# Performance work log

Measured on AMD Instinct MI355X. Metric: run time of the kernel, lower is better.

The kernel has to match this reference:

```python
import jax, jax.numpy as jnp
import numpy as np

OUT_FEATURES = 4096
IN_FEATURES = 4096
NUMEL = OUT_FEATURES * IN_FEATURES          # 16777216
NUM_SUPER = NUMEL // 256                    # 65536 superblocks of 256 weights


def setup_inputs() -> dict:
    key = jax.random.key(0)
    k_x, k_p, k_d, k_dm, k_s, k_m = jax.random.split(key, 6)
    x = jax.random.normal(k_x, (2, 2048, IN_FEATURES), dtype=jnp.float32)
    # packed bytes: two 4-bit quants per byte
    packed = jax.random.randint(k_p, (NUMEL // 2,), 0, 256, dtype=jnp.int32)
    # per-superblock fp scale/min (small positive values like real Q4_K 'd'/'dmin')
    d = jax.random.uniform(k_d, (NUM_SUPER,), dtype=jnp.float32) * 0.02
    dmin = jax.random.uniform(k_dm, (NUM_SUPER,), dtype=jnp.float32) * 0.02
    # per-subblock 6-bit scale/min quants (8 subblocks per superblock)
    scales = jax.random.randint(k_s, (NUM_SUPER * 8,), 0, 64, dtype=jnp.int32)
    mins = jax.random.randint(k_m, (NUM_SUPER * 8,), 0, 64, dtype=jnp.int32)
    return {"x": x, "packed": packed, "d": d, "dmin": dmin,
            "scales": scales, "mins": mins}


def _q4_k_dequantize(packed, d, dmin, scales, mins):
    # nibble split: low then high, interleaved per byte (stack dim=1 + flatten)
    low = packed & 15
    high = (packed >> 4) & 15
    q = jnp.stack([low, high], axis=1).reshape(-1).astype(jnp.float32)  # [NUMEL]
    blocks = q.reshape(NUM_SUPER, 8, 32)
    blk_scale = (scales.astype(jnp.float32) / 63.0).reshape(NUM_SUPER, 8, 1)
    blk_min = (mins.astype(jnp.float32) / 63.0).reshape(NUM_SUPER, 8, 1)
    normalized = blocks / 15.0 * blk_scale + blk_min
    w = normalized * d.reshape(NUM_SUPER, 1, 1) + dmin.reshape(NUM_SUPER, 1, 1)
    return w.reshape(OUT_FEATURES, IN_FEATURES)


def reference(x, packed, d, dmin, scales, mins):
    w = _q4_k_dequantize(packed, d, dmin, scales, mins).astype(x.dtype)
    # F.linear(x, w) = x @ w.T ; bias is None
    return jnp.einsum('bsk,nk->bsn', x, w)
```

## Files before the change

### kernel.cpp

```cpp
#include <hip/hip_runtime.h>
#include <stdint.h>

#define M_DIM 4096
#define K_DIM 4096
#define N_DIM 4096

typedef float f32x4 __attribute__((ext_vector_type(4)));
typedef int   i32x4 __attribute__((ext_vector_type(4)));

__global__ __launch_bounds__(256) void quant_x(const float* __restrict__ x,
                                               int8_t* __restrict__ xq,
                                               float* __restrict__ sx) {
    __shared__ float red[4];
    const int row  = blockIdx.x;
    const int base = threadIdx.x * 16;
    const float* xr = x + (size_t)row * K_DIM + base;
    float4 v[4];
#pragma unroll
    for (int c = 0; c < 4; ++c) v[c] = ((const float4*)xr)[c];
    float am = 0.f;
#pragma unroll
    for (int c = 0; c < 4; ++c) {
        am = fmaxf(am, fabsf(v[c].x)); am = fmaxf(am, fabsf(v[c].y));
        am = fmaxf(am, fabsf(v[c].z)); am = fmaxf(am, fabsf(v[c].w));
    }
#pragma unroll
    for (int off = 32; off; off >>= 1) am = fmaxf(am, __shfl_xor(am, off, 64));
    if ((threadIdx.x & 63) == 0) red[threadIdx.x >> 6] = am;
    __syncthreads();
    float amax = fmaxf(fmaxf(red[0], red[1]), fmaxf(red[2], red[3]));
    amax = fmaxf(amax, 1e-20f);
    const float inv = 127.0f / amax;
    int ow[4];
#pragma unroll
    for (int c = 0; c < 4; ++c) {
        int q0 = __float2int_rn(v[c].x * inv);
        int q1 = __float2int_rn(v[c].y * inv);
        int q2 = __float2int_rn(v[c].z * inv);
        int q3 = __float2int_rn(v[c].w * inv);
        ow[c] = (q0 & 255) | ((q1 & 255) << 8) | ((q2 & 255) << 16) | ((q3 & 255) << 24);
    }
    ((int4*)(xq + (size_t)row * K_DIM + base))[0] = make_int4(ow[0], ow[1], ow[2], ow[3]);
    if (threadIdx.x == 0) sx[row] = amax / 127.0f;
}

__global__ __launch_bounds__(256) void quant_w(const int* __restrict__ packed,
                                               const float* __restrict__ d,
                                               const float* __restrict__ dmin,
                                               const int* __restrict__ scales,
                                               const int* __restrict__ mins,
                                               int8_t* __restrict__ wq,
                                               float* __restrict__ sw) {
    __shared__ float sa[128], sb[128], red[4];
    const int n = blockIdx.x;
    const int t = threadIdx.x;
    float m = 0.f;
    if (t < 128) {
        int sub  = n * 128 + t;
        int sidx = n * 16 + (t >> 3);
        float dd = d[sidx], dm = dmin[sidx];
        float a = dd * (float)scales[sub] * (1.0f / 945.0f);
        float b = dd * (float)mins[sub] * (1.0f / 63.0f) + dm;
        sa[t] = a; sb[t] = b;
        m = 15.0f * a + b;
    }
#pragma unroll
    for (int off = 32; off; off >>= 1) m = fmaxf(m, __shfl_xor(m, off, 64));
    if ((t & 63) == 0) red[t >> 6] = m;
    __syncthreads();
    float rowmax = fmaxf(fmaxf(red[0], red[1]), fmaxf(red[2], red[3]));
    rowmax = fmaxf(rowmax, 1e-20f);
    const float inv = 127.0f / rowmax;

    const int sub = t >> 1;
    const float a = sa[sub] * inv;
    const float b = sb[sub] * inv;
    const int4* p4 = (const int4*)(packed + (size_t)n * (K_DIM / 2) + t * 8);
    int4 pv0 = p4[0], pv1 = p4[1];
    int bytes[8] = {pv0.x, pv0.y, pv0.z, pv0.w, pv1.x, pv1.y, pv1.z, pv1.w};
    int ow[4];
#pragma unroll
    for (int c = 0; c < 4; ++c) {
        int b0 = bytes[2 * c], b1 = bytes[2 * c + 1];
        int q0 = __float2int_rn((float)(b0 & 15) * a + b);
        int q1 = __float2int_rn((float)((b0 >> 4) & 15) * a + b);
        int q2 = __float2int_rn((float)(b1 & 15) * a + b);
        int q3 = __float2int_rn((float)((b1 >> 4) & 15) * a + b);
        ow[c] = (q0 & 255) | ((q1 & 255) << 8) | ((q2 & 255) << 16) | ((q3 & 255) << 24);
    }
    ((int4*)(wq + (size_t)n * K_DIM + t * 16))[0] = make_int4(ow[0], ow[1], ow[2], ow[3]);
    if (t == 0) sw[n] = rowmax / 127.0f;
}

#define BM 128
#define BN 128
#define BKB 64

__device__ __forceinline__ void async_copy16(void* lds, const void* g) {
    __builtin_amdgcn_global_load_lds(
        (const __attribute__((address_space(1))) void*)g,
        (__attribute__((address_space(3))) void*)lds, 16, 0, 0);
}

__global__ __launch_bounds__(256) void gemm_i8(const int8_t* __restrict__ A,
                                               const int8_t* __restrict__ B,
                                               const float* __restrict__ sx,
                                               const float* __restrict__ sw,
                                               float* __restrict__ C) {
    __shared__ int8_t sAb[2][BM * BKB];
    __shared__ int8_t sBb[2][BN * BKB];

    const int tid  = threadIdx.x;
    const int wave = tid >> 6;
    const int lane = tid & 63;
    const int wm = wave >> 1;
    const int wn = wave & 1;
    const int r = lane & 15;
    const int q = lane >> 4;

    const int bid  = blockIdx.x;
    const int xcd  = bid & 7;
    const int slot = bid >> 3;
    const int m0 = (((xcd >> 2) << 4) + (slot & 15)) * BM;
    const int n0 = (((xcd & 3) << 3) + (slot >> 4)) * BN;

    i32x4 acc[4][4] = {};

    const int rowS = tid >> 2;
    const int kcS  = ((lane & 3) ^ ((lane >> 3) & 3)) * 16;
    const int8_t* gA0 = A + (size_t)(m0 + rowS) * K_DIM + kcS;
    const int8_t* gA1 = gA0 + (size_t)64 * K_DIM;
    const int8_t* gB0 = B + (size_t)(n0 + rowS) * K_DIM + kcS;
    const int8_t* gB1 = gB0 + (size_t)64 * K_DIM;
    const int ldsOff = wave * 1024;

    const int fragOff = (4 * r + (q ^ ((r >> 1) & 3))) * 16;

#define STAGE(buf, koff)                                                  \
    do {                                                                  \
        async_copy16(&sAb[buf][ldsOff],        gA0 + (koff));             \
        async_copy16(&sAb[buf][4096 + ldsOff], gA1 + (koff));             \
        async_copy16(&sBb[buf][ldsOff],        gB0 + (koff));             \
        async_copy16(&sBb[buf][4096 + ldsOff], gB1 + (koff));             \
    } while (0)

#define COMPUTE(buf)                                                      \
    do {                                                                  \
        i32x4 af[4], bfr[4];                                              \
        _Pragma("unroll")                                                 \
        for (int tt = 0; tt < 4; ++tt) {                                  \
            af[tt]  = *(const i32x4*)&sAb[buf][(wm * 4 + tt) * 1024 + fragOff]; \
            bfr[tt] = *(const i32x4*)&sBb[buf][(wn * 4 + tt) * 1024 + fragOff]; \
        }                                                                 \
        _Pragma("unroll")                                                 \
        for (int ii = 0; ii < 4; ++ii)                                    \
            _Pragma("unroll")                                             \
            for (int jj = 0; jj < 4; ++jj)                                \
                acc[ii][jj] = __builtin_amdgcn_mfma_i32_16x16x64_i8(      \
                    af[ii], bfr[jj], acc[ii][jj], 0, 0, 0);               \
    } while (0)

    STAGE(0, 0);

#pragma unroll 2
    for (int i = 0; i < 63; ++i) {
        const int cur = i & 1;
        STAGE(cur ^ 1, (i + 1) * BKB);
        asm volatile("s_waitcnt vmcnt(4)" ::: "memory");
        asm volatile("s_barrier" ::: "memory");
        COMPUTE(cur);
        asm volatile("s_waitcnt lgkmcnt(0)" ::: "memory");
        asm volatile("s_barrier" ::: "memory");
    }
    asm volatile("s_waitcnt vmcnt(0)" ::: "memory");
    asm volatile("s_barrier" ::: "memory");
    COMPUTE(1);

#pragma unroll
    for (int i = 0; i < 4; ++i) {
        int row = m0 + wm * 64 + i * 16 + q * 4;
#pragma unroll
        for (int j = 0; j < 4; ++j) {
            int col = n0 + wn * 64 + j * 16 + r;
            float swc = sw[col];
#pragma unroll
            for (int reg = 0; reg < 4; ++reg)
                C[(size_t)(row + reg) * N_DIM + col] =
                    (float)acc[i][j][reg] * sx[row + reg] * swc;
        }
    }
#undef STAGE
#undef COMPUTE
}

extern "C" void kernel_launch(void* const* d_in, const int* in_sizes, int n_in,
                              void* d_out, int out_size, void* d_ws, size_t ws_size,
                              hipStream_t stream) {
    const float* x      = (const float*)d_in[0];
    const int*   packed = (const int*)d_in[1];
    const float* d      = (const float*)d_in[2];
    const float* dmin   = (const float*)d_in[3];
    const int*   scales = (const int*)d_in[4];
    const int*   mins   = (const int*)d_in[5];
    float* out = (float*)d_out;

    int8_t* xq = (int8_t*)d_ws;
    int8_t* wq = xq + (size_t)M_DIM * K_DIM;
    float*  sx = (float*)(wq + (size_t)N_DIM * K_DIM);
    float*  sw = sx + M_DIM;

    quant_x<<<M_DIM, 256, 0, stream>>>(x, xq, sx);
    quant_w<<<N_DIM, 256, 0, stream>>>(packed, d, dmin, scales, mins, wq, sw);
    gemm_i8<<<1024, 256, 0, stream>>>(xq, wq, sx, sw, out);
}
```

Before: 247.4 us.

## Pre-tile int8 operands into MFMA fragment layout and load directly to registers

The quantize kernels now write x and w in a fragment-tiled layout (16 rows by 64 bytes per 1KB tile), so each lane's MFMA operand is a contiguous 16-byte load. The GEMM drops LDS staging and barriers and loads fragments from global memory straight into registers, double-buffered across two register sets. This removes LDS traffic and synchronisation but loses cross-wave sharing in LDS: each wave reloads its A/B fragments from global/L2, roughly doubling cache traffic, and relies on register double-buffering alone to hide latency.

Measured after the change: 270.0 us. 9.1% more time.

```diff
diff --git a/kernel.cpp b/kernel.cpp
--- a/kernel.cpp
+++ b/kernel.cpp
@@ -4,17 +4,19 @@
 #define M_DIM 4096
 #define K_DIM 4096
 #define N_DIM 4096
+#define KT    64
 
 typedef float f32x4 __attribute__((ext_vector_type(4)));
 typedef int   i32x4 __attribute__((ext_vector_type(4)));
+
 
 __global__ __launch_bounds__(256) void quant_x(const float* __restrict__ x,
                                                int8_t* __restrict__ xq,
                                                float* __restrict__ sx) {
     __shared__ float red[4];
     const int row  = blockIdx.x;
-    const int base = threadIdx.x * 16;
-    const float* xr = x + (size_t)row * K_DIM + base;
+    const int t    = threadIdx.x;
+    const float* xr = x + (size_t)row * K_DIM + t * 16;
     float4 v[4];
 #pragma unroll
     for (int c = 0; c < 4; ++c) v[c] = ((const float4*)xr)[c];
@@ -26,7 +28,7 @@
     }
 #pragma unroll
     for (int off = 32; off; off >>= 1) am = fmaxf(am, __shfl_xor(am, off, 64));
-    if ((threadIdx.x & 63) == 0) red[threadIdx.x >> 6] = am;
+    if ((t & 63) == 0) red[t >> 6] = am;
     __syncthreads();
     float amax = fmaxf(fmaxf(red[0], red[1]), fmaxf(red[2], red[3]));
     amax = fmaxf(amax, 1e-20f);
@@ -40,8 +42,10 @@
         int q3 = __float2int_rn(v[c].w * inv);
         ow[c] = (q0 & 255) | ((q1 & 255) << 8) | ((q2 & 255) << 16) | ((q3 & 255) << 24);
     }
-    ((int4*)(xq + (size_t)row * K_DIM + base))[0] = make_int4(ow[0], ow[1], ow[2], ow[3]);
-    if (threadIdx.x == 0) sx[row] = amax / 127.0f;
+    const size_t off = (((size_t)(row >> 4) * KT + (t >> 2)) << 10)
+                     + (((t & 3) << 4) + (row & 15)) * 16;
+    ((int4*)(xq + off))[0] = make_int4(ow[0], ow[1], ow[2], ow[3]);
+    if (t == 0) sx[row] = amax / 127.0f;
 }
 
 __global__ __launch_bounds__(256) void quant_w(const int* __restrict__ packed,
@@ -88,18 +92,10 @@
         int q3 = __float2int_rn((float)((b1 >> 4) & 15) * a + b);
         ow[c] = (q0 & 255) | ((q1 & 255) << 8) | ((q2 & 255) << 16) | ((q3 & 255) << 24);
     }
-    ((int4*)(wq + (size_t)n * K_DIM + t * 16))[0] = make_int4(ow[0], ow[1], ow[2], ow[3]);
+    const size_t off = (((size_t)(n >> 4) * KT + (t >> 2)) << 10)
+                     + (((t & 3) << 4) + (n & 15)) * 16;
+    ((int4*)(wq + off))[0] = make_int4(ow[0], ow[1], ow[2], ow[3]);
     if (t == 0) sw[n] = rowmax / 127.0f;
-}
-
-#define BM 128
-#define BN 128
-#define BKB 64
-
-__device__ __forceinline__ void async_copy16(void* lds, const void* g) {
-    __builtin_amdgcn_global_load_lds(
-        (const __attribute__((address_space(1))) void*)g,
-        (__attribute__((address_space(3))) void*)lds, 16, 0, 0);
 }
 
 __global__ __launch_bounds__(256) void gemm_i8(const int8_t* __restrict__ A,
@@ -107,9 +103,6 @@
                                                const float* __restrict__ sx,
                                                const float* __restrict__ sw,
                                                float* __restrict__ C) {
-    __shared__ int8_t sAb[2][BM * BKB];
-    __shared__ int8_t sBb[2][BN * BKB];
-
     const int tid  = threadIdx.x;
     const int wave = tid >> 6;
     const int lane = tid & 63;
@@ -121,76 +114,63 @@
     const int bid  = blockIdx.x;
     const int xcd  = bid & 7;
     const int slot = bid >> 3;
-    const int m0 = (((xcd >> 2) << 4) + (slot & 15)) * BM;
-    const int n0 = (((xcd & 3) << 3) + (slot >> 4)) * BN;
+    const int m0 = (((xcd >> 2) << 4) + (slot & 15)) * 128;
+    const int n0 = (((xcd & 3) << 3) + (slot >> 4)) * 128;
+
+    const int gA = (m0 >> 4) + wm * 4;
+    const int gB = (n0 >> 4) + wn * 4;
+    const int8_t* pA = A + ((size_t)gA * KT << 10) + lane * 16;
+    const int8_t* pB = B + ((size_t)gB * KT << 10) + lane * 16;
 
     i32x4 acc[4][4] = {};
+    i32x4 a0[4], b0[4], a1[4], b1[4];
 
-    const int rowS = tid >> 2;
-    const int kcS  = ((lane & 3) ^ ((lane >> 3) & 3)) * 16;
-    const int8_t* gA0 = A + (size_t)(m0 + rowS) * K_DIM + kcS;
-    const int8_t* gA1 = gA0 + (size_t)64 * K_DIM;
-    const int8_t* gB0 = B + (size_t)(n0 + rowS) * K_DIM + kcS;
-    const int8_t* gB1 = gB0 + (size_t)64 * K_DIM;
-    const int ldsOff = wave * 1024;
-
-    const int fragOff = (4 * r + (q ^ ((r >> 1) & 3))) * 16;
-
-#define STAGE(buf, koff)                                                  \
-    do {                                                                  \
-        async_copy16(&sAb[buf][ldsOff],        gA0 + (koff));             \
-        async_copy16(&sAb[buf][4096 + ldsOff], gA1 + (koff));             \
-        async_copy16(&sBb[buf][ldsOff],        gB0 + (koff));             \
-        async_copy16(&sBb[buf][4096 + ldsOff], gB1 + (koff));             \
+#define LOADF(fa, fb, i)                                                   \
+    do {                                                                   \
+        _Pragma("unroll")                                                  \
+        for (int tt = 0; tt < 4; ++tt) {                                   \
+            fa[tt] = *(const i32x4*)(pA + ((size_t)(tt * KT + (i)) << 10));\
+            fb[tt] = *(const i32x4*)(pB + ((size_t)(tt * KT + (i)) << 10));\
+        }                                                                  \
     } while (0)
 
-#define COMPUTE(buf)                                                      \
-    do {                                                                  \
-        i32x4 af[4], bfr[4];                                              \
-        _Pragma("unroll")                                                 \
-        for (int tt = 0; tt < 4; ++tt) {                                  \
-            af[tt]  = *(const i32x4*)&sAb[buf][(wm * 4 + tt) * 1024 + fragOff]; \
-            bfr[tt] = *(const i32x4*)&sBb[buf][(wn * 4 + tt) * 1024 + fragOff]; \
-        }                                                                 \
-        _Pragma("unroll")                                                 \
-        for (int ii = 0; ii < 4; ++ii)                                    \
-            _Pragma("unroll")                                             \
-            for (int jj = 0; jj < 4; ++jj)                                \
-                acc[ii][jj] = __builtin_amdgcn_mfma_i32_16x16x64_i8(      \
-                    af[ii], bfr[jj], acc[ii][jj], 0, 0, 0);               \
+#define MFMA(fa, fb)                                                       \
+    do {                                                                   \
+        _Pragma("unroll")                                                  \
+        for (int ii = 0; ii < 4; ++ii)                                     \
+            _Pragma("unroll")                                              \
+            for (int jj = 0; jj < 4; ++jj)                                 \
+                acc[ii][jj] = __builtin_amdgcn_mfma_i32_16x16x64_i8(       \
+                    fa[ii], fb[jj], acc[ii][jj], 0, 0, 0);                 \
     } while (0)
 
-    STAGE(0, 0);
-
-#pragma unroll 2
-    for (int i = 0; i < 63; ++i) {
-        const int cur = i & 1;
-        STAGE(cur ^ 1, (i + 1) * BKB);
-        asm volatile("s_waitcnt vmcnt(4)" ::: "memory");
-        asm volatile("s_barrier" ::: "memory");
-        COMPUTE(cur);
-        asm volatile("s_waitcnt lgkmcnt(0)" ::: "memory");
-        asm volatile("s_barrier" ::: "memory");
+    LOADF(a0, b0, 0);
+#pragma unroll 1
+    for (int i = 0; i < 31; ++i) {
+        LOADF(a1, b1, 2 * i + 1);
+        MFMA(a0, b0);
+        LOADF(a0, b0, 2 * i + 2);
+        MFMA(a1, b1);
     }
-    asm volatile("s_waitcnt vmcnt(0)" ::: "memory");
-    asm volatile("s_barrier" ::: "memory");
-    COMPUTE(1);
+    LOADF(a1, b1, 63);
+    MFMA(a0, b0);
+    MFMA(a1, b1);
+#undef LOADF
+#undef MFMA
 
 #pragma unroll
-    for (int i = 0; i < 4; ++i) {
-        int row = m0 + wm * 64 + i * 16 + q * 4;
+    for (int fi = 0; fi < 4; ++fi) {
+        int row = m0 + wm * 64 + fi * 16 + q * 4;
 #pragma unroll
-        for (int j = 0; j < 4; ++j) {
-            int col = n0 + wn * 64 + j * 16 + r;
+        for (int fj = 0; fj < 4; ++fj) {
+            int col = n0 + wn * 64 + fj * 16 + r;
             float swc = sw[col];
 #pragma unroll
             for (int reg = 0; reg < 4; ++reg)
                 C[(size_t)(row + reg) * N_DIM + col] =
-                    (float)acc[i][j][reg] * sx[row + reg] * swc;
+                    (float)acc[fi][fj][reg] * sx[row + reg] * swc;
         }
     }
-#undef STAGE
-#undef COMPUTE
 }
 
 extern "C" void kernel_launch(void* const* d_in, const int* in_sizes, int n_in,
```
